# Optimization experiments

Hardware: AMD Instinct MI355X
Metric: run time of the kernel (lower is better)

Reference implementation:

```python
import jax, jax.numpy as jnp
import numpy as np
import math

EMBED_DIM = 1024
NUM_HEADS = 16
HEAD_DIM = EMBED_DIM // NUM_HEADS
MAX_POSITION = 1024
BATCH = 4
SEQ_LEN = 1024


def setup_inputs() -> dict:
    key = jax.random.key(0)
    ks = jax.random.split(key, 10)
    s = 1.0 / math.sqrt(EMBED_DIM)
    inp = {
        "x": jax.random.normal(ks[0], (BATCH, SEQ_LEN, EMBED_DIM), dtype=jnp.float32),
        "Wq": jax.random.normal(ks[1], (EMBED_DIM, EMBED_DIM), dtype=jnp.float32) * s,
        "bq": jnp.zeros((EMBED_DIM,), dtype=jnp.float32),
        "Wk": jax.random.normal(ks[2], (EMBED_DIM, EMBED_DIM), dtype=jnp.float32) * s,
        "bk": jnp.zeros((EMBED_DIM,), dtype=jnp.float32),
        "Wv": jax.random.normal(ks[3], (EMBED_DIM, EMBED_DIM), dtype=jnp.float32) * s,
        "bv": jnp.zeros((EMBED_DIM,), dtype=jnp.float32),
        "Wo": jax.random.normal(ks[4], (EMBED_DIM, EMBED_DIM), dtype=jnp.float32) * s,
        "bo": jnp.zeros((EMBED_DIM,), dtype=jnp.float32),
        "rel_key": jax.random.normal(ks[5], (MAX_POSITION, HEAD_DIM), dtype=jnp.float32),
    }
    return inp


def reference(x, Wq, bq, Wk, bk, Wv, bv, Wo, bo, rel_key):
    B, S, E = x.shape
    H, D = NUM_HEADS, HEAD_DIM
    # projections, split heads -> (B, H, S, D)
    Q = (x @ Wq + bq).reshape(B, S, H, D).transpose(0, 2, 1, 3)
    K = (x @ Wk + bk).reshape(B, S, H, D).transpose(0, 2, 1, 3)
    V = (x @ Wv + bv).reshape(B, S, H, D).transpose(0, 2, 1, 3)
    # content scores
    attn_content = jnp.einsum('bhqd,bhkd->bhqk', Q, K)
    # relative-position scores via skew trick
    rel = rel_key[MAX_POSITION - S:, :]              # (S, D)
    QEr = jnp.einsum('bhqd,sd->bhqs', Q, rel)        # (B, H, S, S)
    padded = jnp.pad(QEr, ((0, 0), (0, 0), (0, 0), (1, 0)))  # (B, H, S, S+1)
    Srel = padded.reshape(B, H, S + 1, S)[:, :, 1:, :]       # (B, H, S, S)
    scores = (attn_content + Srel) * (1.0 / math.sqrt(D))
    # causal mask
    mask = jnp.tril(jnp.ones((S, S), dtype=bool))
    scores = jnp.where(mask[None, None], scores, -jnp.inf)
    w = jax.nn.softmax(scores, axis=-1)
    out = jnp.einsum('bhqk,bhkd->bhqd', w, V)
    out = out.transpose(0, 2, 1, 3).reshape(B, S, E)
    return out @ Wo + bo
```

## Files before the change

kernel.cpp:

```cpp
#include <hip/hip_runtime.h>

typedef unsigned short u16;
typedef __attribute__((ext_vector_type(8))) __bf16 bf16x8;
typedef __attribute__((ext_vector_type(4))) float f32x4;
typedef __attribute__((ext_vector_type(4))) u16 u16x4;


__device__ __forceinline__ u16 f2bf(float f) {
  unsigned u = __float_as_uint(f);
  u += 0x7fff + ((u >> 16) & 1);
  return (u16)(u >> 16);
}

__device__ __forceinline__ f32x4 mfma16(bf16x8 a, bf16x8 b, f32x4 c) {
  return __builtin_amdgcn_mfma_f32_16x16x32_bf16(a, b, c, 0, 0, 0);
}

__device__ __forceinline__ void gload16(const void* g, void* l) {
  __builtin_amdgcn_global_load_lds(
      (__attribute__((address_space(1))) unsigned int*)(const_cast<void*>(g)),
      (__attribute__((address_space(3))) unsigned int*)l, 16, 0, 0);
}


__global__ void k_f32_to_bf16(const float* __restrict__ in, u16* __restrict__ out, int n4) {
  int i = blockIdx.x * blockDim.x + threadIdx.x;
  if (i < n4) {
    float4 v = reinterpret_cast<const float4*>(in)[i];
    u16x4 o;
    o.x = f2bf(v.x); o.y = f2bf(v.y); o.z = f2bf(v.z); o.w = f2bf(v.w);
    reinterpret_cast<u16x4*>(out)[i] = o;
  }
}

__global__ void k_prep_small(const float* __restrict__ rel, u16* __restrict__ relb,
                             const float* __restrict__ bq, const float* __restrict__ bk,
                             const float* __restrict__ bv, float* __restrict__ bias) {
  const int bx = blockIdx.x, t = threadIdx.x;
  if (bx < 64) {
    int i = bx * 256 + t;
    float4 v = reinterpret_cast<const float4*>(rel)[i];
    u16x4 o;
    o.x = f2bf(v.x); o.y = f2bf(v.y); o.z = f2bf(v.z); o.w = f2bf(v.w);
    reinterpret_cast<u16x4*>(relb)[i] = o;
  } else {
    int i = (bx - 64) * 256 + t;
    if (i < 3072) bias[i] = (i < 1024) ? bq[i] : (i < 2048 ? bk[i - 1024] : bv[i - 2048]);
  }
}

__global__ void k_transpose_w4(const float* __restrict__ W0, const float* __restrict__ W1,
                               const float* __restrict__ W2, const float* __restrict__ W3,
                               u16* __restrict__ outbase) {
  __shared__ float tile[32][33];
  const int z = blockIdx.z;
  const float* in = (z == 0) ? W0 : (z == 1) ? W1 : (z == 2) ? W2 : W3;
  u16* out = outbase + (size_t)z * 1024 * 1024;
  const int r0 = blockIdx.y * 32, c0 = blockIdx.x * 32;
  const int t = threadIdx.x;
  for (int i = t; i < 1024; i += 256) {
    int r = i >> 5, c = i & 31;
    tile[r][c] = in[(size_t)(r0 + r) * 1024 + c0 + c];
  }
  __syncthreads();
  for (int i = t; i < 1024; i += 256) {
    int r = i >> 5, c = i & 31;
    out[(size_t)(c0 + r) * 1024 + r0 + c] = f2bf(tile[c][r]);
  }
}


template<int MODE>
__global__ __launch_bounds__(256) void k_gemm(
    const u16* __restrict__ A, const u16* __restrict__ B,
    const float* __restrict__ bias, void* __restrict__ Cout,
    u16* __restrict__ Vaux, int M, int N, int Kd)
{
  __shared__ u16 Alds[128 * 64];
  __shared__ u16 Blds[128 * 64];
  const int t = threadIdx.x;
  const int lane = t & 63, wid = t >> 6;
  const int wr = wid >> 1, wc = wid & 1;
  const int l15 = lane & 15, lg = lane >> 4;
  const int m0 = blockIdx.y * 128, n0 = blockIdx.x * 128;

  const f32x4 fzero = {0.f, 0.f, 0.f, 0.f};
  f32x4 acc[4][4];
#pragma unroll
  for (int i = 0; i < 4; i++)
#pragma unroll
    for (int j = 0; j < 4; j++) acc[i][j] = fzero;

  const int srow = t >> 3;
  const int scb  = ((t & 7) * 16) ^ ((srow & 7) << 4);
  const size_t abase = (size_t)(m0 + srow) * Kd + (scb >> 1);
  const size_t bbase = (size_t)(n0 + srow) * Kd + (scb >> 1);

  for (int k0 = 0; k0 < Kd; k0 += 64) {
#pragma unroll
    for (int ci = 0; ci < 4; ci++) {
      gload16(A + abase + (size_t)(32 * ci) * Kd + k0, Alds + (t + 256 * ci) * 8);
      gload16(B + bbase + (size_t)(32 * ci) * Kd + k0, Blds + (t + 256 * ci) * 8);
    }
    __syncthreads();
#pragma unroll
    for (int kk = 0; kk < 2; kk++) {
      bf16x8 av[4], bv[4];
#pragma unroll
      for (int mi = 0; mi < 4; mi++) {
        const int row = wr * 64 + mi * 16 + l15;
        av[mi] = *reinterpret_cast<const bf16x8*>(
            (const char*)Alds + row * 128 + ((kk * 64 + lg * 16) ^ ((row & 7) << 4)));
      }
#pragma unroll
      for (int ni = 0; ni < 4; ni++) {
        const int row = wc * 64 + ni * 16 + l15;
        bv[ni] = *reinterpret_cast<const bf16x8*>(
            (const char*)Blds + row * 128 + ((kk * 64 + lg * 16) ^ ((row & 7) << 4)));
      }
#pragma unroll
      for (int mi = 0; mi < 4; mi++)
#pragma unroll
        for (int ni = 0; ni < 4; ni++)
          acc[mi][ni] = mfma16(av[mi], bv[ni], acc[mi][ni]);
    }
    __syncthreads();
  }

#pragma unroll
  for (int mi = 0; mi < 4; mi++) {
#pragma unroll
    for (int ni = 0; ni < 4; ni++) {
      const int col = n0 + wc * 64 + ni * 16 + l15;
      const float bcol = bias[col];
#pragma unroll
      for (int r = 0; r < 4; r++) {
        const int row = m0 + wr * 64 + mi * 16 + lg * 4 + r;
        const float v = acc[mi][ni][r] + bcol;
        if (MODE == 0) {
          ((float*)Cout)[(size_t)row * N + col] = v;
        } else {
          if (col < 2048) {
            ((u16*)Cout)[(size_t)row * N + col] = f2bf(v);
          } else {
            const int bb = row >> 10, ss = row & 1023;
            Vaux[((size_t)bb * 1024 + (col - 2048)) * 1024 + ss] = f2bf(v);
          }
        }
      }
    }
  }
}


__global__ __launch_bounds__(256, 4) void k_attn(
    const u16* __restrict__ qkv,
    const u16* __restrict__ vt,
    const u16* __restrict__ relb,
    u16* __restrict__ Oout)
{
  __shared__ u16 Klds[64 * 64];
  __shared__ u16 Vlds[64 * 64];
  __shared__ float Sbuf[4][16 * 84];

  const int t = threadIdx.x;
  const int lane = t & 63, w = t >> 6;
  const int l15 = lane & 15, lg = lane >> 4;
  const int blk = blockIdx.x;
  const int bh = blk & 63;
  const int g = blk >> 6;
  const int jq = g >> 2, rq = g & 3;
  const int qbt = (jq == 0) ? (15 - rq) : (jq == 1) ? (8 + rq) : (jq == 2) ? (7 - rq) : rq;
  const int b = bh >> 4, h = bh & 15;
  const int qb = qbt * 64;
  const int qw = qb + w * 16;

  float* Wb = Sbuf[w];
  u16* Pb = (u16*)Sbuf[w];

  const f32x4 fzero = {0.f, 0.f, 0.f, 0.f};

  const size_t qrow = (size_t)(b * 1024 + qw + l15) * 3072 + h * 64;
  bf16x8 aQ0 = *reinterpret_cast<const bf16x8*>(qkv + qrow + lg * 8);
  bf16x8 aQ1 = *reinterpret_cast<const bf16x8*>(qkv + qrow + 32 + lg * 8);

  f32x4 oacc[4];
  float l_r[4];
#pragma unroll
  for (int r = 0; r < 4; r++) { oacc[r] = fzero; l_r[r] = 0.f; }

  const int srow = t >> 3;
  const int scb = ((t & 7) * 16) ^ ((srow & 7) << 4);
  const u16* Ks0 = qkv + (size_t)(b * 1024 + srow) * 3072 + 1024 + h * 64 + (scb >> 1);
  const u16* Ks1 = Ks0 + 32 * 3072;
  const u16* Vs0 = vt + (size_t)(bh * 64 + srow) * 1024 + (scb >> 1);
  const u16* Vs1 = Vs0 + 32 * 1024;
  u16* Kd0 = Klds + t * 8;  u16* Kd1 = Klds + (t + 256) * 8;
  u16* Vd0 = Vlds + t * 8;  u16* Vd1 = Vlds + (t + 256) * 8;

  const int nk = qbt + 1;
  const float SC = 0.125f * 1.44269504f;

  for (int kt = 0; kt < nk; kt++) {
    const int k0 = kt * 64;
    gload16(Ks0 + (size_t)k0 * 3072, Kd0);
    gload16(Ks1 + (size_t)k0 * 3072, Kd1);
    gload16(Vs0 + k0, Vd0);
    gload16(Vs1 + k0, Vd1);
    __syncthreads();

    f32x4 sc4[4];
#pragma unroll
    for (int tt = 0; tt < 4; tt++) sc4[tt] = fzero;
#pragma unroll
    for (int tt = 0; tt < 4; tt++) {
      const int row = tt * 16 + l15;
      const int sw = (row & 7) << 4;
      bf16x8 b0 = *reinterpret_cast<const bf16x8*>((const char*)Klds + row * 128 + ((lg * 16) ^ sw));
      bf16x8 b1 = *reinterpret_cast<const bf16x8*>((const char*)Klds + row * 128 + ((64 + lg * 16) ^ sw));
      sc4[tt] = mfma16(aQ0, b0, sc4[tt]);
      sc4[tt] = mfma16(aQ1, b1, sc4[tt]);
    }

    const int rbase = 1008 + k0 - qw;
#pragma unroll
    for (int wj = 0; wj < 5; wj++) {
      int rr = rbase + wj * 16 + l15;
      rr = rr < 0 ? 0 : (rr > 1023 ? 1023 : rr);
      const u16* rp = relb + rr * 64;
      bf16x8 b0 = *reinterpret_cast<const bf16x8*>(rp + lg * 8);
      bf16x8 b1 = *reinterpret_cast<const bf16x8*>(rp + 32 + lg * 8);
      f32x4 z = fzero;
      z = mfma16(aQ0, b0, z);
      z = mfma16(aQ1, b1, z);
#pragma unroll
      for (int r = 0; r < 4; r++)
        Wb[(lg * 4 + r) * 84 + wj * 16 + l15] = z[r];
    }
    __builtin_amdgcn_wave_barrier();

    float pvv[4][4];
#pragma unroll
    for (int r = 0; r < 4; r++) {
      const int rowi = lg * 4 + r;
      const int q = qw + rowi;
      const float* wrow = Wb + rowi * 84 + (15 - rowi);
#pragma unroll
      for (int tt = 0; tt < 4; tt++) {
        const int kg = k0 + tt * 16 + l15;
        float s = (sc4[tt][r] + wrow[tt * 16 + l15]) * SC;
        s = (kg <= q) ? s : -1e30f;
        float p = exp2f(s);
        pvv[tt][r] = p;
        l_r[r] += p;
      }
    }
    __builtin_amdgcn_wave_barrier();
    asm volatile("" ::: "memory");

#pragma unroll
    for (int tt = 0; tt < 4; tt++)
#pragma unroll
      for (int r = 0; r < 4; r++) {
        const int rowi = lg * 4 + r;
        const int cb = (32 * tt + 2 * l15) ^ ((rowi & 7) << 4);
        *(u16*)((char*)Pb + rowi * 128 + cb) = f2bf(pvv[tt][r]);
      }
    __builtin_amdgcn_wave_barrier();

#pragma unroll
    for (int s = 0; s < 2; s++) {
      const int acb = (s * 64 + lg * 16) ^ ((l15 & 7) << 4);
      bf16x8 aP = *reinterpret_cast<const bf16x8*>((const char*)Pb + l15 * 128 + acb);
#pragma unroll
      for (int dt = 0; dt < 4; dt++) {
        const int vrow = dt * 16 + l15;
        const int vcb = (s * 64 + lg * 16) ^ ((vrow & 7) << 4);
        bf16x8 bV = *reinterpret_cast<const bf16x8*>((const char*)Vlds + vrow * 128 + vcb);
        oacc[dt] = mfma16(aP, bV, oacc[dt]);
      }
    }
    __syncthreads();
  }

#pragma unroll
  for (int r = 0; r < 4; r++) {
    float l = l_r[r];
#pragma unroll
    for (int xm = 1; xm < 16; xm <<= 1) l += __shfl_xor(l, xm);
    const float inv = 1.f / l;
    const int q = qw + lg * 4 + r;
#pragma unroll
    for (int dt = 0; dt < 4; dt++)
      Oout[(size_t)(b * 1024 + q) * 1024 + h * 64 + dt * 16 + l15] = f2bf(oacc[dt][r] * inv);
  }
}


extern "C" void kernel_launch(void* const* d_in, const int* in_sizes, int n_in,
                              void* d_out, int out_size, void* d_ws, size_t ws_size,
                              hipStream_t stream) {
  const float* x   = (const float*)d_in[0];
  const float* Wq  = (const float*)d_in[1];
  const float* bq  = (const float*)d_in[2];
  const float* Wk  = (const float*)d_in[3];
  const float* bk  = (const float*)d_in[4];
  const float* Wv  = (const float*)d_in[5];
  const float* bv  = (const float*)d_in[6];
  const float* Wo  = (const float*)d_in[7];
  const float* bo  = (const float*)d_in[8];
  const float* rel = (const float*)d_in[9];

  const size_t MB = 1024 * 1024;
  char* ws = (char*)d_ws;
  u16*   xb    = (u16*)(ws);
  u16*   Wt    = (u16*)(ws + 8 * MB);
  u16*   qkvb  = (u16*)(ws + 16 * MB);
  u16*   vtb   = (u16*)(ws + 40 * MB);
  u16*   relbb = (u16*)(ws + 48 * MB);
  float* bqkv  = (float*)(ws + 49 * MB);
  u16*   Ob    = xb;

  k_f32_to_bf16<<<4096, 256, 0, stream>>>(x, xb, 1048576);
  k_prep_small<<<76, 256, 0, stream>>>(rel, relbb, bq, bk, bv, bqkv);
  k_transpose_w4<<<dim3(32, 32, 4), 256, 0, stream>>>(Wq, Wk, Wv, Wo, Wt);

  k_gemm<2><<<dim3(24, 32), 256, 0, stream>>>(xb, Wt, bqkv, qkvb, vtb, 4096, 3072, 1024);

  k_attn<<<1024, 256, 0, stream>>>(qkvb, vtb, relbb, Ob);

  k_gemm<0><<<dim3(8, 32), 256, 0, stream>>>(Ob, Wt + 3 * MB, bo, d_out, nullptr, 4096, 1024, 1024);
}
```

Measured before the change: 140.3 us.

## Merge prep kernels, narrow output GEMM tile, prefetch rel-key fragments in attention

Folds the three preprocessing kernels (x cast, weight transpose, rel/bias prep) into one launch to cut launch overhead. Makes the GEMM's N tile a template parameter and runs the output projection with 64-wide tiles, doubling its block count so more CUs are used. In the attention kernel, the rel-key fragment loads are moved before the K/V tile load and barrier so their global latency overlaps with the copy. This costs more registers in attention and gives less reuse per block in the output GEMM.

Measured after the change: 139.0 us. Within noise of the previous version (-0.9%).

```diff
diff --git a/kernel.cpp b/kernel.cpp
--- a/kernel.cpp
+++ b/kernel.cpp
@@ -23,73 +23,70 @@
 }
 
 
-__global__ void k_f32_to_bf16(const float* __restrict__ in, u16* __restrict__ out, int n4) {
-  int i = blockIdx.x * blockDim.x + threadIdx.x;
-  if (i < n4) {
-    float4 v = reinterpret_cast<const float4*>(in)[i];
+__global__ void k_prep_all(const float* __restrict__ x, u16* __restrict__ xb,
+                           const float* __restrict__ W0, const float* __restrict__ W1,
+                           const float* __restrict__ W2, const float* __restrict__ W3,
+                           u16* __restrict__ Wt,
+                           const float* __restrict__ rel, u16* __restrict__ relb,
+                           const float* __restrict__ bq, const float* __restrict__ bk,
+                           const float* __restrict__ bv, float* __restrict__ bias) {
+  __shared__ float tile[32][33];
+  const int bx = blockIdx.x, t = threadIdx.x;
+  if (bx < 4096) {
+    int i = bx * 256 + t;
+    float4 v = reinterpret_cast<const float4*>(x)[i];
     u16x4 o;
     o.x = f2bf(v.x); o.y = f2bf(v.y); o.z = f2bf(v.z); o.w = f2bf(v.w);
-    reinterpret_cast<u16x4*>(out)[i] = o;
-  }
-}
-
-__global__ void k_prep_small(const float* __restrict__ rel, u16* __restrict__ relb,
-                             const float* __restrict__ bq, const float* __restrict__ bk,
-                             const float* __restrict__ bv, float* __restrict__ bias) {
-  const int bx = blockIdx.x, t = threadIdx.x;
-  if (bx < 64) {
-    int i = bx * 256 + t;
+    reinterpret_cast<u16x4*>(xb)[i] = o;
+  } else if (bx < 8192) {
+    const int id = bx - 4096;
+    const int z = id >> 10;
+    const float* in = (z == 0) ? W0 : (z == 1) ? W1 : (z == 2) ? W2 : W3;
+    u16* out = Wt + (size_t)z * 1024 * 1024;
+    const int r0 = ((id >> 5) & 31) * 32, c0 = (id & 31) * 32;
+    for (int i = t; i < 1024; i += 256) {
+      int r = i >> 5, c = i & 31;
+      tile[r][c] = in[(size_t)(r0 + r) * 1024 + c0 + c];
+    }
+    __syncthreads();
+    for (int i = t; i < 1024; i += 256) {
+      int r = i >> 5, c = i & 31;
+      out[(size_t)(c0 + r) * 1024 + r0 + c] = f2bf(tile[c][r]);
+    }
+  } else if (bx < 8256) {
+    int i = (bx - 8192) * 256 + t;
     float4 v = reinterpret_cast<const float4*>(rel)[i];
     u16x4 o;
     o.x = f2bf(v.x); o.y = f2bf(v.y); o.z = f2bf(v.z); o.w = f2bf(v.w);
     reinterpret_cast<u16x4*>(relb)[i] = o;
   } else {
-    int i = (bx - 64) * 256 + t;
+    int i = (bx - 8256) * 256 + t;
     if (i < 3072) bias[i] = (i < 1024) ? bq[i] : (i < 2048 ? bk[i - 1024] : bv[i - 2048]);
   }
 }
 
-__global__ void k_transpose_w4(const float* __restrict__ W0, const float* __restrict__ W1,
-                               const float* __restrict__ W2, const float* __restrict__ W3,
-                               u16* __restrict__ outbase) {
-  __shared__ float tile[32][33];
-  const int z = blockIdx.z;
-  const float* in = (z == 0) ? W0 : (z == 1) ? W1 : (z == 2) ? W2 : W3;
-  u16* out = outbase + (size_t)z * 1024 * 1024;
-  const int r0 = blockIdx.y * 32, c0 = blockIdx.x * 32;
-  const int t = threadIdx.x;
-  for (int i = t; i < 1024; i += 256) {
-    int r = i >> 5, c = i & 31;
-    tile[r][c] = in[(size_t)(r0 + r) * 1024 + c0 + c];
-  }
-  __syncthreads();
-  for (int i = t; i < 1024; i += 256) {
-    int r = i >> 5, c = i & 31;
-    out[(size_t)(c0 + r) * 1024 + r0 + c] = f2bf(tile[c][r]);
-  }
-}
-
-
-template<int MODE>
+
+template<int MODE, int BN>
 __global__ __launch_bounds__(256) void k_gemm(
     const u16* __restrict__ A, const u16* __restrict__ B,
     const float* __restrict__ bias, void* __restrict__ Cout,
     u16* __restrict__ Vaux, int M, int N, int Kd)
 {
+  constexpr int NF = BN / 32;
   __shared__ u16 Alds[128 * 64];
-  __shared__ u16 Blds[128 * 64];
+  __shared__ u16 Blds[BN * 64];
   const int t = threadIdx.x;
   const int lane = t & 63, wid = t >> 6;
   const int wr = wid >> 1, wc = wid & 1;
   const int l15 = lane & 15, lg = lane >> 4;
-  const int m0 = blockIdx.y * 128, n0 = blockIdx.x * 128;
+  const int m0 = blockIdx.y * 128, n0 = blockIdx.x * BN;
 
   const f32x4 fzero = {0.f, 0.f, 0.f, 0.f};
-  f32x4 acc[4][4];
+  f32x4 acc[4][NF];
 #pragma unroll
   for (int i = 0; i < 4; i++)
 #pragma unroll
-    for (int j = 0; j < 4; j++) acc[i][j] = fzero;
+    for (int j = 0; j < NF; j++) acc[i][j] = fzero;
 
   const int srow = t >> 3;
   const int scb  = ((t & 7) * 16) ^ ((srow & 7) << 4);
@@ -98,14 +95,15 @@
 
   for (int k0 = 0; k0 < Kd; k0 += 64) {
 #pragma unroll
-    for (int ci = 0; ci < 4; ci++) {
+    for (int ci = 0; ci < 4; ci++)
       gload16(A + abase + (size_t)(32 * ci) * Kd + k0, Alds + (t + 256 * ci) * 8);
+#pragma unroll
+    for (int ci = 0; ci < NF; ci++)
       gload16(B + bbase + (size_t)(32 * ci) * Kd + k0, Blds + (t + 256 * ci) * 8);
-    }
     __syncthreads();
 #pragma unroll
     for (int kk = 0; kk < 2; kk++) {
-      bf16x8 av[4], bv[4];
+      bf16x8 av[4], bv[NF];
 #pragma unroll
       for (int mi = 0; mi < 4; mi++) {
         const int row = wr * 64 + mi * 16 + l15;
@@ -113,15 +111,15 @@
             (const char*)Alds + row * 128 + ((kk * 64 + lg * 16) ^ ((row & 7) << 4)));
       }
 #pragma unroll
-      for (int ni = 0; ni < 4; ni++) {
-        const int row = wc * 64 + ni * 16 + l15;
+      for (int ni = 0; ni < NF; ni++) {
+        const int row = wc * (BN / 2) + ni * 16 + l15;
         bv[ni] = *reinterpret_cast<const bf16x8*>(
             (const char*)Blds + row * 128 + ((kk * 64 + lg * 16) ^ ((row & 7) << 4)));
       }
 #pragma unroll
       for (int mi = 0; mi < 4; mi++)
 #pragma unroll
-        for (int ni = 0; ni < 4; ni++)
+        for (int ni = 0; ni < NF; ni++)
           acc[mi][ni] = mfma16(av[mi], bv[ni], acc[mi][ni]);
     }
     __syncthreads();
@@ -130,8 +128,8 @@
 #pragma unroll
   for (int mi = 0; mi < 4; mi++) {
 #pragma unroll
-    for (int ni = 0; ni < 4; ni++) {
-      const int col = n0 + wc * 64 + ni * 16 + l15;
+    for (int ni = 0; ni < NF; ni++) {
+      const int col = n0 + wc * (BN / 2) + ni * 16 + l15;
       const float bcol = bias[col];
 #pragma unroll
       for (int r = 0; r < 4; r++) {
@@ -203,6 +201,18 @@
 
   for (int kt = 0; kt < nk; kt++) {
     const int k0 = kt * 64;
+
+    const int rbase = 1008 + k0 - qw;
+    bf16x8 rb0[5], rb1[5];
+#pragma unroll
+    for (int wj = 0; wj < 5; wj++) {
+      int rr = rbase + wj * 16 + l15;
+      rr = rr < 0 ? 0 : (rr > 1023 ? 1023 : rr);
+      const u16* rp = relb + rr * 64;
+      rb0[wj] = *reinterpret_cast<const bf16x8*>(rp + lg * 8);
+      rb1[wj] = *reinterpret_cast<const bf16x8*>(rp + 32 + lg * 8);
+    }
+
     gload16(Ks0 + (size_t)k0 * 3072, Kd0);
     gload16(Ks1 + (size_t)k0 * 3072, Kd1);
     gload16(Vs0 + k0, Vd0);
@@ -222,17 +232,11 @@
       sc4[tt] = mfma16(aQ1, b1, sc4[tt]);
     }
 
-    const int rbase = 1008 + k0 - qw;
 #pragma unroll
     for (int wj = 0; wj < 5; wj++) {
-      int rr = rbase + wj * 16 + l15;
-      rr = rr < 0 ? 0 : (rr > 1023 ? 1023 : rr);
-      const u16* rp = relb + rr * 64;
-      bf16x8 b0 = *reinterpret_cast<const bf16x8*>(rp + lg * 8);
-      bf16x8 b1 = *reinterpret_cast<const bf16x8*>(rp + 32 + lg * 8);
       f32x4 z = fzero;
-      z = mfma16(aQ0, b0, z);
-      z = mfma16(aQ1, b1, z);
+      z = mfma16(aQ0, rb0[wj], z);
+      z = mfma16(aQ1, rb1[wj], z);
 #pragma unroll
       for (int r = 0; r < 4; r++)
         Wb[(lg * 4 + r) * 84 + wj * 16 + l15] = z[r];
@@ -321,13 +325,11 @@
   float* bqkv  = (float*)(ws + 49 * MB);
   u16*   Ob    = xb;
 
-  k_f32_to_bf16<<<4096, 256, 0, stream>>>(x, xb, 1048576);
-  k_prep_small<<<76, 256, 0, stream>>>(rel, relbb, bq, bk, bv, bqkv);
-  k_transpose_w4<<<dim3(32, 32, 4), 256, 0, stream>>>(Wq, Wk, Wv, Wo, Wt);
-
-  k_gemm<2><<<dim3(24, 32), 256, 0, stream>>>(xb, Wt, bqkv, qkvb, vtb, 4096, 3072, 1024);
+  k_prep_all<<<8268, 256, 0, stream>>>(x, xb, Wq, Wk, Wv, Wo, Wt, rel, relbb, bq, bk, bv, bqkv);
+
+  k_gemm<2, 128><<<dim3(24, 32), 256, 0, stream>>>(xb, Wt, bqkv, qkvb, vtb, 4096, 3072, 1024);
 
   k_attn<<<1024, 256, 0, stream>>>(qkvb, vtb, relbb, Ob);
 
-  k_gemm<0><<<dim3(8, 32), 256, 0, stream>>>(Ob, Wt + 3 * MB, bo, d_out, nullptr, 4096, 1024, 1024);
-}
+  k_gemm<0, 64><<<dim3(16, 32), 256, 0, stream>>>(Ob, Wt + 3 * MB, bo, d_out, nullptr, 4096, 1024, 1024);
+}
```
